# Kernel tuning notes

Hardware: AMD Instinct MI355X
Metric: run time of the kernel (lower is better)

The kernel has to match this reference:

```python
import jax, jax.numpy as jnp
import numpy as np

N = 50000      # nodes
E = 800000     # edges (avg degree 16)
DF = 128       # node feature dim
EF = 16        # edge feature dim
EH = 64        # edge_filters
NH = 128       # node_filters
C = 40         # classes


def setup_inputs() -> dict:
    key = jax.random.key(0)
    ks = jax.random.split(key, 11)
    s = lambda fan_in: 1.0 / np.sqrt(fan_in)
    return {
        "x": jax.random.normal(ks[0], (N, DF), jnp.float32),
        "edge_feat": jax.random.normal(ks[1], (E, EF), jnp.float32),
        "W1": jax.random.normal(ks[2], (EF, EH), jnp.float32) * s(EF),
        "b1": jnp.zeros((EH,), jnp.float32),
        "W2": jax.random.normal(ks[3], (EH, 1), jnp.float32) * s(EH),
        "b2": jnp.zeros((1,), jnp.float32),
        "Wc1": jax.random.normal(ks[4], (DF, NH), jnp.float32) * s(DF),
        "bc1": jnp.zeros((NH,), jnp.float32),
        "Wc2": jax.random.normal(ks[5], (NH, C), jnp.float32) * s(NH),
        "bc2": jnp.zeros((C,), jnp.float32),
        "edge_index": jax.random.randint(ks[6], (2, E), 0, N, jnp.int32),
    }


def reference(x, edge_feat, W1, b1, W2, b2, Wc1, bc1, Wc2, bc2, edge_index):
    # Edge MLP: per-edge scalar weight in (0, 1)
    eh = jnp.maximum(edge_feat @ W1 + b1, 0.0)          # [E, EH] relu
    ew = jax.nn.sigmoid(eh @ W2 + b2)[:, 0]             # [E]

    # SparseTensor(edges.T, ew, (n, n)): indices are (row=dst, col=src)
    dst = edge_index[0]
    src = edge_index[1]

    # GCNConv 1: relu(A @ (x @ Wc1) + bc1)
    h = x @ Wc1                                         # [N, NH]
    msg = h[src] * ew[:, None]                          # [E, NH] gather
    agg = jax.ops.segment_sum(msg, dst, num_segments=N) # [N, NH] scatter
    h1 = jnp.maximum(agg + bc1, 0.0)
    # dropout(training=False) is identity

    # GCNConv 2: A @ (h1 @ Wc2) + bc2 (linear activation)
    h2 = h1 @ Wc2                                       # [N, C]
    msg2 = h2[src] * ew[:, None]                        # [E, C]
    agg2 = jax.ops.segment_sum(msg2, dst, num_segments=N) + bc2

    return -jax.nn.log_softmax(agg2, axis=1)            # [N, C]
```

## Files before the change

kernel.cpp:

```cpp
#include <hip/hip_runtime.h>
#include <math.h>

#define N_NODES 50000
#define N_EDGES 800000
#define DF 128
#define EF 16
#define EH 64
#define NH 128
#define NC 40
#define NCP 64
#define SCAN_B 196

typedef __attribute__((ext_vector_type(8))) short short8v;
typedef __attribute__((ext_vector_type(4))) short short4v;

__device__ __forceinline__ float bf2f(unsigned short u) {
    union { unsigned int i; float f; } c; c.i = ((unsigned int)u) << 16; return c.f;
}
__device__ __forceinline__ unsigned short f2bf(float f) {
    union { float f; unsigned int i; } c; c.f = f;
    unsigned int r = c.i + 0x7FFFu + ((c.i >> 16) & 1u);
    return (unsigned short)(r >> 16);
}
__device__ __forceinline__ float rdlane(float v, int lane) {
    return __int_as_float(__builtin_amdgcn_readlane(__float_as_int(v), lane));
}

__global__ __launch_bounds__(256) void edge_mlp_kernel(
    const float* __restrict__ ef, const float* __restrict__ W1,
    const float* __restrict__ b1, const float* __restrict__ W2,
    const float* __restrict__ b2, const int* __restrict__ dst,
    float* __restrict__ ew, int* __restrict__ deg)
{
    __shared__ float4 W1s4[EF * 16];
    __shared__ float4 b1s4[16];
    __shared__ float4 W2s4[16];
    int t = threadIdx.x;
    for (int i = t; i < EF * 16; i += 256) W1s4[i] = ((const float4*)W1)[i];
    if (t < 16) { b1s4[t] = ((const float4*)b1)[t]; W2s4[t] = ((const float4*)W2)[t]; }
    __syncthreads();

    int e = blockIdx.x * 256 + t;
    if (e >= N_EDGES) return;

    float f[EF];
    const float4* ef4 = (const float4*)(ef + (long)e * EF);
    #pragma unroll
    for (int i = 0; i < 4; ++i) {
        float4 v = ef4[i];
        f[4*i+0] = v.x; f[4*i+1] = v.y; f[4*i+2] = v.z; f[4*i+3] = v.w;
    }
    float s = 0.f;
    #pragma unroll 4
    for (int jc = 0; jc < 16; ++jc) {
        float4 a = b1s4[jc];
        #pragma unroll
        for (int k = 0; k < EF; ++k) {
            float4 w = W1s4[k * 16 + jc];
            a.x += f[k] * w.x; a.y += f[k] * w.y;
            a.z += f[k] * w.z; a.w += f[k] * w.w;
        }
        float4 w2 = W2s4[jc];
        s += fmaxf(a.x, 0.f) * w2.x + fmaxf(a.y, 0.f) * w2.y
           + fmaxf(a.z, 0.f) * w2.z + fmaxf(a.w, 0.f) * w2.w;
    }
    s += b2[0];
    ew[e] = 1.f / (1.f + expf(-s));
    atomicAdd(&deg[dst[e]], 1);
}

__global__ __launch_bounds__(256) void gemm1_kernel(
    const float* __restrict__ x, const float* __restrict__ Wc1,
    unsigned short* __restrict__ hb)
{
    __shared__ float xs[64][DF];
    int t = threadIdx.x;
    long r0 = (long)blockIdx.x * 64;
    for (int i = t; i < 64 * (DF / 4); i += 256) {
        int r = i >> 5, kq = i & 31;
        long rr = r0 + r;
        float4 v = (rr < N_NODES) ? *(const float4*)(x + rr * DF + kq * 4)
                                  : make_float4(0.f, 0.f, 0.f, 0.f);
        *(float4*)(&xs[r][kq * 4]) = v;
    }
    __syncthreads();

    int tr = t >> 5;
    int tc = t & 31;
    float acc[8][4];
    #pragma unroll
    for (int i = 0; i < 8; ++i)
        #pragma unroll
        for (int j = 0; j < 4; ++j) acc[i][j] = 0.f;

    for (int k = 0; k < DF; k += 4) {
        float4 w0 = *(const float4*)(Wc1 + (k + 0) * NH + tc * 4);
        float4 w1 = *(const float4*)(Wc1 + (k + 1) * NH + tc * 4);
        float4 w2 = *(const float4*)(Wc1 + (k + 2) * NH + tc * 4);
        float4 w3 = *(const float4*)(Wc1 + (k + 3) * NH + tc * 4);
        #pragma unroll
        for (int i = 0; i < 8; ++i) {
            float4 xv = *(const float4*)(&xs[tr * 8 + i][k]);
            acc[i][0] += xv.x * w0.x + xv.y * w1.x + xv.z * w2.x + xv.w * w3.x;
            acc[i][1] += xv.x * w0.y + xv.y * w1.y + xv.z * w2.y + xv.w * w3.y;
            acc[i][2] += xv.x * w0.z + xv.y * w1.z + xv.z * w2.z + xv.w * w3.z;
            acc[i][3] += xv.x * w0.w + xv.y * w1.w + xv.z * w2.w + xv.w * w3.w;
        }
    }
    #pragma unroll
    for (int i = 0; i < 8; ++i) {
        long r = r0 + tr * 8 + i;
        if (r < N_NODES) {
            ushort4 sv;
            sv.x = f2bf(acc[i][0]); sv.y = f2bf(acc[i][1]);
            sv.z = f2bf(acc[i][2]); sv.w = f2bf(acc[i][3]);
            *(ushort4*)(hb + r * NH + tc * 4) = sv;
        }
    }
}

__global__ __launch_bounds__(256) void scan_part_kernel(
    const int* __restrict__ deg, int* __restrict__ bsum)
{
    __shared__ int red[256];
    int t = threadIdx.x;
    int n = blockIdx.x * 256 + t;
    red[t] = (n < N_NODES) ? deg[n] : 0;
    __syncthreads();
    for (int o = 128; o > 0; o >>= 1) {
        if (t < o) red[t] += red[t + o];
        __syncthreads();
    }
    if (t == 0) bsum[blockIdx.x] = red[0];
}

__global__ __launch_bounds__(256) void scan_top_kernel(
    const int* __restrict__ bsum, int* __restrict__ boff)
{
    __shared__ int s[256];
    int t = threadIdx.x;
    s[t] = (t < SCAN_B) ? bsum[t] : 0;
    __syncthreads();
    for (int o = 1; o < 256; o <<= 1) {
        int v = (t >= o) ? s[t - o] : 0;
        __syncthreads();
        s[t] += v;
        __syncthreads();
    }
    if (t < SCAN_B) boff[t] = (t == 0) ? 0 : s[t - 1];
}

__global__ __launch_bounds__(256) void scan_write_kernel(
    const int* __restrict__ deg, const int* __restrict__ boff,
    int* __restrict__ rowptr)
{
    __shared__ int s[256];
    int t = threadIdx.x;
    int n = blockIdx.x * 256 + t;
    int v = (n < N_NODES) ? deg[n] : 0;
    s[t] = v;
    __syncthreads();
    for (int o = 1; o < 256; o <<= 1) {
        int u = (t >= o) ? s[t - o] : 0;
        __syncthreads();
        s[t] += u;
        __syncthreads();
    }
    if (n < N_NODES) rowptr[n] = boff[blockIdx.x] + s[t] - v;
}

__global__ __launch_bounds__(256) void fill_csr_kernel(
    const int* __restrict__ dst, const int* __restrict__ src,
    const float* __restrict__ ew, int* __restrict__ rowptr,
    int2* __restrict__ csr)
{
    int e = blockIdx.x * 256 + threadIdx.x;
    if (e >= N_EDGES) return;
    int p = atomicAdd(&rowptr[dst[e]], 1);
    csr[p] = make_int2(src[e], __float_as_int(ew[e]));
}

__global__ __launch_bounds__(256) void wc2t_kernel(
    const float* __restrict__ Wc2, float* __restrict__ Wc2T)
{
    for (int i = threadIdx.x; i < NH * NC; i += 256) {
        int k = i / NC, c = i - k * NC;
        Wc2T[c * NH + k] = Wc2[i];
    }
}

__global__ __launch_bounds__(256) void gather1_gemm2_kernel(
    const unsigned short* __restrict__ hb, const int* __restrict__ rp_end,
    const int2* __restrict__ csr, const float* __restrict__ bc1,
    const float* __restrict__ Wc2T, unsigned short* __restrict__ h2b)
{
    int t = threadIdx.x;
    int node = blockIdx.x * 4 + (t >> 6);
    int lane = t & 63;
    int l16 = lane & 15, g = lane >> 4;

    int end   = rp_end[node];
    int start = (node == 0) ? 0 : rp_end[node - 1];

    float acc[8];
    #pragma unroll
    for (int i = 0; i < 8; ++i) acc[i] = 0.f;

    for (int base = start; base < end; base += 64) {
        int n = end - base; if (n > 64) n = 64;
        int s = 0; float w = 0.f;
        if (lane < n) {
            int2 p = csr[base + lane];
            s = p.x; w = __int_as_float(p.y);
        }
        #pragma unroll 4
        for (int j = 0; j * 4 < n; ++j) {
            int idx = j * 4 + g;
            int   sj = __shfl(s, idx, 64);
            float wj = __shfl(w, idx, 64);
            short8v hv = *(const short8v*)(hb + (long)sj * NH + l16 * 8);
            #pragma unroll
            for (int i = 0; i < 8; ++i)
                acc[i] += wj * bf2f((unsigned short)hv[i]);
        }
    }
    #pragma unroll
    for (int i = 0; i < 8; ++i) {
        acc[i] += __shfl_xor(acc[i], 16, 64);
        acc[i] += __shfl_xor(acc[i], 32, 64);
    }
    float4 b0 = *(const float4*)(bc1 + l16 * 8);
    float4 b1 = *(const float4*)(bc1 + l16 * 8 + 4);
    float h1v[8];
    h1v[0] = fmaxf(acc[0] + b0.x, 0.f); h1v[1] = fmaxf(acc[1] + b0.y, 0.f);
    h1v[2] = fmaxf(acc[2] + b0.z, 0.f); h1v[3] = fmaxf(acc[3] + b0.w, 0.f);
    h1v[4] = fmaxf(acc[4] + b1.x, 0.f); h1v[5] = fmaxf(acc[5] + b1.y, 0.f);
    h1v[6] = fmaxf(acc[6] + b1.z, 0.f); h1v[7] = fmaxf(acc[7] + b1.w, 0.f);

    int c = (lane < NC) ? lane : (NC - 1);
    const float4* wrow = (const float4*)(Wc2T + c * NH);
    float o = 0.f;
    #pragma unroll
    for (int kq = 0; kq < 32; ++kq) {
        float4 wv = wrow[kq];
        if ((kq & 1) == 0) {
            o += rdlane(h1v[0], kq >> 1) * wv.x + rdlane(h1v[1], kq >> 1) * wv.y
               + rdlane(h1v[2], kq >> 1) * wv.z + rdlane(h1v[3], kq >> 1) * wv.w;
        } else {
            o += rdlane(h1v[4], kq >> 1) * wv.x + rdlane(h1v[5], kq >> 1) * wv.y
               + rdlane(h1v[6], kq >> 1) * wv.z + rdlane(h1v[7], kq >> 1) * wv.w;
        }
    }
    h2b[(long)node * NCP + lane] = f2bf((lane < NC) ? o : 0.f);
}

__global__ __launch_bounds__(256) void gather2_lsm_kernel(
    const unsigned short* __restrict__ h2b, const int* __restrict__ rp_end,
    const int2* __restrict__ csr, const float* __restrict__ bc2,
    float* __restrict__ out)
{
    int t = threadIdx.x;
    int node = blockIdx.x * 4 + (t >> 6);
    int lane = t & 63;
    int l16 = lane & 15, g = lane >> 4;

    int end   = rp_end[node];
    int start = (node == 0) ? 0 : rp_end[node - 1];

    float acc[4];
    #pragma unroll
    for (int i = 0; i < 4; ++i) acc[i] = 0.f;

    for (int base = start; base < end; base += 64) {
        int n = end - base; if (n > 64) n = 64;
        int s = 0; float w = 0.f;
        if (lane < n) {
            int2 p = csr[base + lane];
            s = p.x; w = __int_as_float(p.y);
        }
        #pragma unroll 4
        for (int j = 0; j * 4 < n; ++j) {
            int idx = j * 4 + g;
            int   sj = __shfl(s, idx, 64);
            float wj = __shfl(w, idx, 64);
            short4v hv = *(const short4v*)(h2b + (long)sj * NCP + l16 * 4);
            #pragma unroll
            for (int i = 0; i < 4; ++i)
                acc[i] += wj * bf2f((unsigned short)hv[i]);
        }
    }
    #pragma unroll
    for (int i = 0; i < 4; ++i) {
        acc[i] += __shfl_xor(acc[i], 16, 64);
        acc[i] += __shfl_xor(acc[i], 32, 64);
    }

    bool valid = (l16 < 10);
    float4 bcv = valid ? *(const float4*)(bc2 + l16 * 4) : make_float4(0.f, 0.f, 0.f, 0.f);
    float v[4];
    v[0] = acc[0] + bcv.x; v[1] = acc[1] + bcv.y;
    v[2] = acc[2] + bcv.z; v[3] = acc[3] + bcv.w;

    float mx = valid ? fmaxf(fmaxf(v[0], v[1]), fmaxf(v[2], v[3])) : -INFINITY;
    #pragma unroll
    for (int o = 1; o <= 8; o <<= 1) mx = fmaxf(mx, __shfl_xor(mx, o, 64));
    float se = 0.f;
    if (valid) se = expf(v[0]-mx) + expf(v[1]-mx) + expf(v[2]-mx) + expf(v[3]-mx);
    #pragma unroll
    for (int o = 1; o <= 8; o <<= 1) se += __shfl_xor(se, o, 64);
    float lse = mx + logf(se);

    if (valid && g == 0) {
        float4 r = make_float4(lse - v[0], lse - v[1], lse - v[2], lse - v[3]);
        *(float4*)(out + (long)node * NC + l16 * 4) = r;
    }
}

extern "C" void kernel_launch(void* const* d_in, const int* in_sizes, int n_in,
                              void* d_out, int out_size, void* d_ws, size_t ws_size,
                              hipStream_t stream)
{
    const float* x         = (const float*)d_in[0];
    const float* edge_feat = (const float*)d_in[1];
    const float* W1        = (const float*)d_in[2];
    const float* b1        = (const float*)d_in[3];
    const float* W2        = (const float*)d_in[4];
    const float* b2        = (const float*)d_in[5];
    const float* Wc1       = (const float*)d_in[6];
    const float* bc1       = (const float*)d_in[7];
    const float* Wc2       = (const float*)d_in[8];
    const float* bc2       = (const float*)d_in[9];
    const int*   eidx      = (const int*)d_in[10];
    const int*   dst = eidx;
    const int*   src = eidx + N_EDGES;
    float* out = (float*)d_out;

    float*          ew     = (float*)d_ws;
    unsigned short* hb     = (unsigned short*)(ew + N_EDGES);
    unsigned short* h2b    = hb + (long)N_NODES * NH;
    int2*           csr    = (int2*)(h2b + (long)N_NODES * NCP);
    int*            deg    = (int*)(csr + N_EDGES);
    int*            rowptr = deg + N_NODES;
    int*            bsum   = rowptr + N_NODES;
    int*            boff   = bsum + 256;
    float*          Wc2T   = (float*)(boff + 256);

    hipMemsetAsync(deg, 0, sizeof(int) * (size_t)N_NODES, stream);

    edge_mlp_kernel<<<(N_EDGES + 255) / 256, 256, 0, stream>>>(
        edge_feat, W1, b1, W2, b2, dst, ew, deg);
    gemm1_kernel<<<(N_NODES + 63) / 64, 256, 0, stream>>>(x, Wc1, hb);
    scan_part_kernel<<<SCAN_B, 256, 0, stream>>>(deg, bsum);
    scan_top_kernel<<<1, 256, 0, stream>>>(bsum, boff);
    scan_write_kernel<<<SCAN_B, 256, 0, stream>>>(deg, boff, rowptr);
    wc2t_kernel<<<1, 256, 0, stream>>>(Wc2, Wc2T);
    fill_csr_kernel<<<(N_EDGES + 255) / 256, 256, 0, stream>>>(
        dst, src, ew, rowptr, csr);
    gather1_gemm2_kernel<<<N_NODES / 4, 256, 0, stream>>>(
        hb, rowptr, csr, bc1, Wc2T, h2b);
    gather2_lsm_kernel<<<N_NODES / 4, 256, 0, stream>>>(
        h2b, rowptr, csr, bc2, out);
}
```

Measured before the change: 429.5 us.

## Compute edge MLP with bf16 MFMA and drop Wc2 transpose kernel

The per-edge MLP now runs on matrix cores: each wave loads 64 edges' features as bf16 fragments and does 16x16x32 MFMAs against W1 held in registers, then reduces the relu·W2 products with lane shuffles and writes sigmoid weights four at a time. This replaces scalar FMA loops over LDS-staged weights. The separate Wc2 transpose kernel is removed, and the second GEMM reads Wc2 directly with shuffles in place of readlane. Inputs are rounded to bf16 in the edge MLP, which lowers precision of edge weights.

```diff
diff --git a/kernel.cpp b/kernel.cpp
--- a/kernel.cpp
+++ b/kernel.cpp
@@ -13,6 +13,7 @@
 
 typedef __attribute__((ext_vector_type(8))) short short8v;
 typedef __attribute__((ext_vector_type(4))) short short4v;
+typedef __attribute__((ext_vector_type(4))) float f32x4;
 
 __device__ __forceinline__ float bf2f(unsigned short u) {
     union { unsigned int i; float f; } c; c.i = ((unsigned int)u) << 16; return c.f;
@@ -21,9 +22,6 @@
     union { float f; unsigned int i; } c; c.f = f;
     unsigned int r = c.i + 0x7FFFu + ((c.i >> 16) & 1u);
     return (unsigned short)(r >> 16);
-}
-__device__ __forceinline__ float rdlane(float v, int lane) {
-    return __int_as_float(__builtin_amdgcn_readlane(__float_as_int(v), lane));
 }
 
 __global__ __launch_bounds__(256) void edge_mlp_kernel(
@@ -32,41 +30,70 @@
     const float* __restrict__ b2, const int* __restrict__ dst,
     float* __restrict__ ew, int* __restrict__ deg)
 {
-    __shared__ float4 W1s4[EF * 16];
-    __shared__ float4 b1s4[16];
-    __shared__ float4 W2s4[16];
-    int t = threadIdx.x;
-    for (int i = t; i < EF * 16; i += 256) W1s4[i] = ((const float4*)W1)[i];
-    if (t < 16) { b1s4[t] = ((const float4*)b1)[t]; W2s4[t] = ((const float4*)W2)[t]; }
-    __syncthreads();
-
-    int e = blockIdx.x * 256 + t;
-    if (e >= N_EDGES) return;
-
-    float f[EF];
-    const float4* ef4 = (const float4*)(ef + (long)e * EF);
-    #pragma unroll
-    for (int i = 0; i < 4; ++i) {
-        float4 v = ef4[i];
-        f[4*i+0] = v.x; f[4*i+1] = v.y; f[4*i+2] = v.z; f[4*i+3] = v.w;
-    }
-    float s = 0.f;
-    #pragma unroll 4
-    for (int jc = 0; jc < 16; ++jc) {
-        float4 a = b1s4[jc];
+    int t = threadIdx.x;
+    int lane = t & 63;
+    int wv = t >> 6;
+    int l15 = lane & 15, kg = lane >> 4;
+
+    short8v Bf[4];
+    float b1v[4], w2v[4];
+    #pragma unroll
+    for (int tt = 0; tt < 4; ++tt) {
+        int col = tt * 16 + l15;
+        short8v bv = {0, 0, 0, 0, 0, 0, 0, 0};
+        if (kg < 2) {
+            #pragma unroll
+            for (int i = 0; i < 8; ++i)
+                bv[i] = (short)f2bf(W1[(kg * 8 + i) * EH + col]);
+        }
+        Bf[tt] = bv;
+        b1v[tt] = b1[col];
+        w2v[tt] = W2[col];
+    }
+    float b2s = b2[0];
+
+    long e0w = ((long)blockIdx.x * 4 + wv) * 64;
+
+    #pragma unroll
+    for (int rt = 0; rt < 4; ++rt) {
+        long e0 = e0w + rt * 16;
+        short8v Af = {0, 0, 0, 0, 0, 0, 0, 0};
+        if (kg < 2) {
+            const float4* p = (const float4*)(ef + (e0 + l15) * EF + kg * 8);
+            float4 v0 = p[0], v1 = p[1];
+            Af[0] = (short)f2bf(v0.x); Af[1] = (short)f2bf(v0.y);
+            Af[2] = (short)f2bf(v0.z); Af[3] = (short)f2bf(v0.w);
+            Af[4] = (short)f2bf(v1.x); Af[5] = (short)f2bf(v1.y);
+            Af[6] = (short)f2bf(v1.z); Af[7] = (short)f2bf(v1.w);
+        }
+        f32x4 a0 = {0.f, 0.f, 0.f, 0.f}, a1 = a0, a2 = a0, a3 = a0;
+        a0 = __builtin_amdgcn_mfma_f32_16x16x32_bf16(Af, Bf[0], a0, 0, 0, 0);
+        a1 = __builtin_amdgcn_mfma_f32_16x16x32_bf16(Af, Bf[1], a1, 0, 0, 0);
+        a2 = __builtin_amdgcn_mfma_f32_16x16x32_bf16(Af, Bf[2], a2, 0, 0, 0);
+        a3 = __builtin_amdgcn_mfma_f32_16x16x32_bf16(Af, Bf[3], a3, 0, 0, 0);
+
+        float s[4];
         #pragma unroll
-        for (int k = 0; k < EF; ++k) {
-            float4 w = W1s4[k * 16 + jc];
-            a.x += f[k] * w.x; a.y += f[k] * w.y;
-            a.z += f[k] * w.z; a.w += f[k] * w.w;
-        }
-        float4 w2 = W2s4[jc];
-        s += fmaxf(a.x, 0.f) * w2.x + fmaxf(a.y, 0.f) * w2.y
-           + fmaxf(a.z, 0.f) * w2.z + fmaxf(a.w, 0.f) * w2.w;
-    }
-    s += b2[0];
-    ew[e] = 1.f / (1.f + expf(-s));
-    atomicAdd(&deg[dst[e]], 1);
+        for (int r = 0; r < 4; ++r) {
+            s[r] = fmaxf(a0[r] + b1v[0], 0.f) * w2v[0]
+                 + fmaxf(a1[r] + b1v[1], 0.f) * w2v[1]
+                 + fmaxf(a2[r] + b1v[2], 0.f) * w2v[2]
+                 + fmaxf(a3[r] + b1v[3], 0.f) * w2v[3];
+            s[r] += __shfl_xor(s[r], 1, 64);
+            s[r] += __shfl_xor(s[r], 2, 64);
+            s[r] += __shfl_xor(s[r], 4, 64);
+            s[r] += __shfl_xor(s[r], 8, 64);
+        }
+        if (l15 == 0) {
+            float4 sg;
+            sg.x = 1.f / (1.f + expf(-(s[0] + b2s)));
+            sg.y = 1.f / (1.f + expf(-(s[1] + b2s)));
+            sg.z = 1.f / (1.f + expf(-(s[2] + b2s)));
+            sg.w = 1.f / (1.f + expf(-(s[3] + b2s)));
+            *(float4*)(ew + e0 + kg * 4) = sg;
+        }
+    }
+    atomicAdd(&deg[dst[e0w + lane]], 1);
 }
 
 __global__ __launch_bounds__(256) void gemm1_kernel(
@@ -180,19 +207,10 @@
     csr[p] = make_int2(src[e], __float_as_int(ew[e]));
 }
 
-__global__ __launch_bounds__(256) void wc2t_kernel(
-    const float* __restrict__ Wc2, float* __restrict__ Wc2T)
-{
-    for (int i = threadIdx.x; i < NH * NC; i += 256) {
-        int k = i / NC, c = i - k * NC;
-        Wc2T[c * NH + k] = Wc2[i];
-    }
-}
-
 __global__ __launch_bounds__(256) void gather1_gemm2_kernel(
     const unsigned short* __restrict__ hb, const int* __restrict__ rp_end,
     const int2* __restrict__ csr, const float* __restrict__ bc1,
-    const float* __restrict__ Wc2T, unsigned short* __restrict__ h2b)
+    const float* __restrict__ Wc2, unsigned short* __restrict__ h2b)
 {
     int t = threadIdx.x;
     int node = blockIdx.x * 4 + (t >> 6);
@@ -238,18 +256,11 @@
     h1v[6] = fmaxf(acc[6] + b1.z, 0.f); h1v[7] = fmaxf(acc[7] + b1.w, 0.f);
 
     int c = (lane < NC) ? lane : (NC - 1);
-    const float4* wrow = (const float4*)(Wc2T + c * NH);
     float o = 0.f;
-    #pragma unroll
-    for (int kq = 0; kq < 32; ++kq) {
-        float4 wv = wrow[kq];
-        if ((kq & 1) == 0) {
-            o += rdlane(h1v[0], kq >> 1) * wv.x + rdlane(h1v[1], kq >> 1) * wv.y
-               + rdlane(h1v[2], kq >> 1) * wv.z + rdlane(h1v[3], kq >> 1) * wv.w;
-        } else {
-            o += rdlane(h1v[4], kq >> 1) * wv.x + rdlane(h1v[5], kq >> 1) * wv.y
-               + rdlane(h1v[6], kq >> 1) * wv.z + rdlane(h1v[7], kq >> 1) * wv.w;
-        }
+    #pragma unroll 8
+    for (int k = 0; k < NH; ++k) {
+        float hk = __shfl(h1v[k & 7], k >> 3, 64);
+        o += hk * Wc2[k * NC + c];
     }
     h2b[(long)node * NCP + lane] = f2bf((lane < NC) ? o : 0.f);
 }
@@ -343,21 +354,19 @@
     int*            rowptr = deg + N_NODES;
     int*            bsum   = rowptr + N_NODES;
     int*            boff   = bsum + 256;
-    float*          Wc2T   = (float*)(boff + 256);
 
     hipMemsetAsync(deg, 0, sizeof(int) * (size_t)N_NODES, stream);
 
-    edge_mlp_kernel<<<(N_EDGES + 255) / 256, 256, 0, stream>>>(
+    edge_mlp_kernel<<<N_EDGES / 256, 256, 0, stream>>>(
         edge_feat, W1, b1, W2, b2, dst, ew, deg);
     gemm1_kernel<<<(N_NODES + 63) / 64, 256, 0, stream>>>(x, Wc1, hb);
     scan_part_kernel<<<SCAN_B, 256, 0, stream>>>(deg, bsum);
     scan_top_kernel<<<1, 256, 0, stream>>>(bsum, boff);
     scan_write_kernel<<<SCAN_B, 256, 0, stream>>>(deg, boff, rowptr);
-    wc2t_kernel<<<1, 256, 0, stream>>>(Wc2, Wc2T);
     fill_csr_kernel<<<(N_EDGES + 255) / 256, 256, 0, stream>>>(
         dst, src, ew, rowptr, csr);
     gather1_gemm2_kernel<<<N_NODES / 4, 256, 0, stream>>>(
-        hb, rowptr, csr, bc1, Wc2T, h2b);
+        hb, rowptr, csr, bc1, Wc2, h2b);
     gather2_lsm_kernel<<<N_NODES / 4, 256, 0, stream>>>(
         h2b, rowptr, csr, bc2, out);
 }
```

After: 350.5 us. -18.4%, faster.
